# Kernel tuning notes

Hardware: AMD Instinct MI355X
Metric: run time of the kernel (lower is better)

The kernel has to match this reference:

```python
import jax, jax.numpy as jnp
import numpy as np

Z = 128          # z_size
K = 16           # number of objects
B = 2048         # batch size
DIM = 2 * Z      # 256


def _lin_init(k, out_dim, in_dim):
    bound = 1.0 / np.sqrt(in_dim)
    kw, kb = jax.random.split(k)
    W = jax.random.uniform(kw, (out_dim, in_dim), minval=-bound, maxval=bound, dtype=jnp.float32)
    b = jax.random.uniform(kb, (out_dim,), minval=-bound, maxval=bound, dtype=jnp.float32)
    return W, b


def setup_inputs() -> dict:
    key = jax.random.key(0)
    ks = jax.random.split(key, 12)
    W_obj, b_obj = _lin_init(ks[2], DIM, Z)            # d_obj: z_size -> dim
    Wih, bih = _lin_init(ks[3], 3 * Z, DIM)            # GRU input weights (dim -> z_size hidden)
    Whh, bhh = _lin_init(ks[4], 3 * Z, Z)              # GRU hidden weights
    We, be = _lin_init(ks[5], 2 * DIM, 2 * DIM)        # d_obj_eff: 512 -> 512
    Wa, ba = _lin_init(ks[6], 1, 2 * DIM)              # d_obj_att: 512 -> 1
    Wc, bc = _lin_init(ks[7], Z, DIM + 2 * DIM)        # d_comb: 768 -> z_size
    Wl, bl = _lin_init(ks[8], Z, Z)                    # loc
    Ws, bs = _lin_init(ks[9], Z, Z)                    # scale
    Wh, bh = _lin_init(ks[10], Z, Z)                   # h projection (RSSM)
    return {
        'z': jax.random.normal(ks[0], (B * K, Z), dtype=jnp.float32),
        'h0': jax.random.normal(ks[1], (B * K, Z), dtype=jnp.float32),
        'W_obj': W_obj, 'b_obj': b_obj,
        'Wih': Wih, 'bih': bih, 'Whh': Whh, 'bhh': bhh,
        'We': We, 'be': be, 'Wa': Wa, 'ba': ba,
        'Wc': Wc, 'bc': bc, 'Wl': Wl, 'bl': bl,
        'Ws': Ws, 'bs': bs, 'Wh': Wh, 'bh': bh,
    }


def _gru_step(x, h, Wih, Whh, bih, bhh):
    # torch nn.GRU single step, 1 layer
    gi = x @ Wih.T + bih
    gh = h @ Whh.T + bhh
    i_r, i_z, i_n = jnp.split(gi, 3, axis=-1)
    h_r, h_z, h_n = jnp.split(gh, 3, axis=-1)
    r = jax.nn.sigmoid(i_r + h_r)
    u = jax.nn.sigmoid(i_z + h_z)
    n = jnp.tanh(i_n + r * h_n)
    return (1.0 - u) * n + u * h


def reference(z, h0, W_obj, b_obj, Wih, bih, Whh, bhh, We, be, Wa, ba, Wc, bc, Wl, bl, Ws, bs, Wh, bh):
    # 1) object embedding
    z_embed = jax.nn.elu(z @ W_obj.T + b_obj)                      # [B*K, DIM]
    # 2) RSSM: one GRU step; output of step == new hidden for 1-layer GRU
    h_new = _gru_step(z_embed, h0, Wih, Whh, bih, bhh)             # [B*K, Z]
    ze = h_new.reshape(B, K, Z)
    z_emb = jnp.concatenate([ze, ze], axis=2)                      # [B, K, DIM] (output and hidden are identical)
    # 3) all unordered pairs i<j; effects are reused symmetrically
    ii, jj = np.triu_indices(K, k=1)                               # P = K*(K-1)/2 pairs
    zed = jnp.concatenate([z_emb[:, ii], z_emb[:, jj]], axis=-1)   # [B, P, 2*DIM]
    eff = jax.nn.elu(zed @ We.T + be)                              # [B, P, 2*DIM]
    att = jax.nn.sigmoid(eff @ Wa.T + ba)                          # [B, P, 1]
    w = att * eff                                                  # [B, P, 2*DIM]
    # 4) attention-weighted scatter-sum of effects to both endpoints
    E = jnp.zeros((B, K, 2 * DIM), dtype=w.dtype)
    E = E.at[:, ii].add(w).at[:, jj].add(w)                        # [B, K, 2*DIM]
    # 5) combine and project
    rel = (jnp.concatenate([z_emb, E], axis=-1) @ Wc.T + bc).reshape(B * K, Z)
    loc = rel @ Wl.T + bl
    scale = rel @ Ws.T + bs
    h_out = rel @ Wh.T + bh
    return (jnp.concatenate([loc, scale], axis=1), h_out)
```

## Files before the change

kernel.cpp:

```cpp
#include <hip/hip_runtime.h>


typedef __attribute__((ext_vector_type(8))) short bf16x8;
typedef __attribute__((ext_vector_type(4))) float f32x4;

__device__ __forceinline__ float fast_exp(float x) { return __expf(x); }
__device__ __forceinline__ float eluf(float x) {
  return x > 0.0f ? x : fast_exp(x) - 1.0f;
}
__device__ __forceinline__ float sigmoidf_(float x) {
  return __builtin_amdgcn_rcpf(1.0f + fast_exp(-x));
}
__device__ __forceinline__ float tanhf_(float x) {
  return 1.0f - 2.0f * __builtin_amdgcn_rcpf(fast_exp(2.0f * x) + 1.0f);
}
__device__ __forceinline__ short f2bf(float x) {
  unsigned u = __builtin_bit_cast(unsigned, x);
  unsigned r = (u + 0x7FFFu + ((u >> 16) & 1u)) >> 16;
  return (short)r;
}
__device__ __forceinline__ float bf2f(short s) {
  return __builtin_bit_cast(float, ((unsigned)(unsigned short)s) << 16);
}

__global__ __launch_bounds__(256) void prep_kernel(
    const float* __restrict__ We, const float* __restrict__ Wc,
    const float* __restrict__ Wl, const float* __restrict__ Wsc,
    const float* __restrict__ Wh, const float* __restrict__ bl,
    const float* __restrict__ bs, const float* __restrict__ bh,
    const float* __restrict__ W_obj, const float* __restrict__ Wih,
    const float* __restrict__ Whh,
    float* __restrict__ blsh, short* __restrict__ WUV2_bf,
    short* __restrict__ Wrel_bf, short* __restrict__ Wlsh_bf,
    short* __restrict__ Wobj_bf, short* __restrict__ Wih_bf,
    short* __restrict__ Whh_bf)
{
  int idx = blockIdx.x * 256 + threadIdx.x;
  if (idx < 131072) {
    int o = idx >> 7, d = idx & 127;
    float v;
    if (o < 512) v = We[o * 512 + d] + We[o * 512 + d + 128];
    else { int oo = o - 512; v = We[oo * 512 + d + 256] + We[oo * 512 + d + 384]; }
    WUV2_bf[idx] = f2bf(v);
  } else if (idx < 212992) {
    int j = idx - 131072; int o = j / 640, c = j - o * 640;
    float v = (c < 128) ? (Wc[o * 768 + c] + Wc[o * 768 + c + 128])
                        : Wc[o * 768 + c + 128];
    Wrel_bf[j] = f2bf(v);
  } else if (idx < 262144) {
    int j = idx - 212992; int o = j >> 7, c = j & 127;
    float v = (o < 128) ? Wl[o * 128 + c]
            : (o < 256) ? Wsc[(o - 128) * 128 + c]
                        : Wh[(o - 256) * 128 + c];
    Wlsh_bf[j] = f2bf(v);
  } else if (idx < 262528) {
    int j = idx - 262144;
    blsh[j] = (j < 128) ? bl[j] : (j < 256) ? bs[j - 128] : bh[j - 256];
  } else if (idx < 295296) {
    int j = idx - 262528; Wobj_bf[j] = f2bf(W_obj[j]);
  } else if (idx < 393600) {
    int j = idx - 295296; Wih_bf[j] = f2bf(Wih[j]);
  } else if (idx < 442752) {
    int j = idx - 393600; Whh_bf[j] = f2bf(Whh[j]);
  }
}

__global__ __launch_bounds__(256) void cvt_zh_kernel(
    const float* __restrict__ z, const float* __restrict__ h0,
    short* __restrict__ z_bf, short* __restrict__ h0_bf)
{
  int g = blockIdx.x * 256 + threadIdx.x;
  const float* src; short* dst; int off;
  if (g < 1048576) { src = z;  dst = z_bf;  off = g << 2; }
  else             { src = h0; dst = h0_bf; off = (g - 1048576) << 2; }
  float4 v = *(const float4*)(src + off);
  short4 o;
  o.x = f2bf(v.x); o.y = f2bf(v.y); o.z = f2bf(v.z); o.w = f2bf(v.w);
  *(short4*)(dst + off) = o;
}

template<int ACT, int OUTMODE, int HASBIAS>
__global__ __launch_bounds__(256) void mfma_gemm(
    const short* __restrict__ A, int lda, int K,
    const short* __restrict__ W,
    const float* __restrict__ bias,
    float* __restrict__ C, int ldc,
    short* __restrict__ Cb,
    float* __restrict__ C2)
{
  const int t = threadIdx.x;
  const int wv = t >> 6, l = t & 63;
  const int lr = l & 15, lk = l >> 4;
  const int row0 = blockIdx.x * 64 + wv * 16;
  const int col0 = blockIdx.y * 64;

  const short* Ap = A + (size_t)(row0 + lr) * lda + lk * 8;
  const short* Wp = W + (size_t)(col0 + lr) * K + lk * 8;
  const size_t wstep = (size_t)16 * K;

  f32x4 acc0 = {0.f,0.f,0.f,0.f}, acc1 = {0.f,0.f,0.f,0.f};
  f32x4 acc2 = {0.f,0.f,0.f,0.f}, acc3 = {0.f,0.f,0.f,0.f};
  for (int k0 = 0; k0 < K; k0 += 32) {
    bf16x8 a  = *(const bf16x8*)(Ap + k0);
    bf16x8 b0 = *(const bf16x8*)(Wp + k0);
    bf16x8 b1 = *(const bf16x8*)(Wp + wstep + k0);
    bf16x8 b2 = *(const bf16x8*)(Wp + 2 * wstep + k0);
    bf16x8 b3 = *(const bf16x8*)(Wp + 3 * wstep + k0);
    acc0 = __builtin_amdgcn_mfma_f32_16x16x32_bf16(a, b0, acc0, 0, 0, 0);
    acc1 = __builtin_amdgcn_mfma_f32_16x16x32_bf16(a, b1, acc1, 0, 0, 0);
    acc2 = __builtin_amdgcn_mfma_f32_16x16x32_bf16(a, b2, acc2, 0, 0, 0);
    acc3 = __builtin_amdgcn_mfma_f32_16x16x32_bf16(a, b3, acc3, 0, 0, 0);
  }
  f32x4 accs[4] = {acc0, acc1, acc2, acc3};
#pragma unroll
  for (int ct = 0; ct < 4; ++ct) {
    const int c = col0 + ct * 16 + lr;
    const float bv = HASBIAS ? bias[c] : 0.0f;
#pragma unroll
    for (int j = 0; j < 4; ++j) {
      const int r = row0 + lk * 4 + j;
      float x = accs[ct][j] + bv;
      if (ACT == 1) x = eluf(x);
      if (OUTMODE == 0) {
        C[(size_t)r * ldc + c] = x;
      } else if (OUTMODE == 1) {
        Cb[(size_t)r * ldc + c] = f2bf(x);
      } else {
        if (c < 256) C[(size_t)r * 256 + c] = x;
        else         C2[(size_t)r * 128 + (c - 256)] = x;
      }
    }
  }
}

__global__ __launch_bounds__(256) void gru_gates_kernel(
    const float* __restrict__ gi, const float* __restrict__ gh,
    const float* __restrict__ h0, short* __restrict__ Acat)
{
  int g = blockIdx.x * 256 + threadIdx.x;
  int r = g >> 5, c = (g & 31) << 2;
  const float* gir = gi + (size_t)r * 384;
  const float* ghr = gh + (size_t)r * 384;
  float4 ir  = *(const float4*)(gir + c);
  float4 iz  = *(const float4*)(gir + 128 + c);
  float4 in_ = *(const float4*)(gir + 256 + c);
  float4 hr  = *(const float4*)(ghr + c);
  float4 hz  = *(const float4*)(ghr + 128 + c);
  float4 hn  = *(const float4*)(ghr + 256 + c);
  float4 h   = *(const float4*)(h0 + (size_t)r * 128 + c);
  float4 o;
  {
    float rg = sigmoidf_(ir.x + hr.x), u = sigmoidf_(iz.x + hz.x);
    float n = tanhf_(in_.x + rg * hn.x);
    o.x = (1.f - u) * n + u * h.x;
  }
  {
    float rg = sigmoidf_(ir.y + hr.y), u = sigmoidf_(iz.y + hz.y);
    float n = tanhf_(in_.y + rg * hn.y);
    o.y = (1.f - u) * n + u * h.y;
  }
  {
    float rg = sigmoidf_(ir.z + hr.z), u = sigmoidf_(iz.z + hz.z);
    float n = tanhf_(in_.z + rg * hn.z);
    o.z = (1.f - u) * n + u * h.z;
  }
  {
    float rg = sigmoidf_(ir.w + hr.w), u = sigmoidf_(iz.w + hz.w);
    float n = tanhf_(in_.w + rg * hn.w);
    o.w = (1.f - u) * n + u * h.w;
  }
  short4 o4;
  o4.x = f2bf(o.x); o4.y = f2bf(o.y); o4.z = f2bf(o.z); o4.w = f2bf(o.w);
  *(short4*)(Acat + (size_t)r * 640 + c) = o4;
}

__global__ __launch_bounds__(512) void pair2_kernel(
    short* __restrict__ Acat,
    const float* __restrict__ UV_all,
    const float* __restrict__ be, const float* __restrict__ Wa,
    const float* __restrict__ ba)
{
  __shared__ float UV[16 * 1024];
  const int b = blockIdx.x, t = threadIdx.x;
  const int w = t >> 6, l = t & 63;

  {
    const float4* src = (const float4*)(UV_all + (size_t)b * 16384);
    float4* dst = (float4*)UV;
#pragma unroll
    for (int i = 0; i < 8; ++i) dst[t + i * 512] = src[t + i * 512];
  }
  float4 beA = *(const float4*)(be + (l << 2));
  float4 beB = *(const float4*)(be + 256 + (l << 2));
  float4 waA = *(const float4*)(Wa + (l << 2));
  float4 waB = *(const float4*)(Wa + 256 + (l << 2));
  const float ba0 = ba[0];
  __syncthreads();

#pragma unroll
  for (int kk = 0; kk < 2; ++kk) {
    const int k = (w << 1) + kk;
    float accA[4] = {0.f, 0.f, 0.f, 0.f};
    float accB[4] = {0.f, 0.f, 0.f, 0.f};
#pragma unroll 1
    for (int m = 0; m < 16; ++m) {
      if (m == k) continue;
      int i = k < m ? k : m;
      int j = k < m ? m : k;
      const float* Ui = &UV[i * 1024 + (l << 2)];
      const float* Vj = &UV[j * 1024 + 512 + (l << 2)];
      float4 u0 = *(const float4*)Ui;
      float4 u1 = *(const float4*)(Ui + 256);
      float4 v0 = *(const float4*)Vj;
      float4 v1 = *(const float4*)(Vj + 256);
      float eA[4], eB[4];
      eA[0] = eluf(u0.x + v0.x + beA.x);
      eA[1] = eluf(u0.y + v0.y + beA.y);
      eA[2] = eluf(u0.z + v0.z + beA.z);
      eA[3] = eluf(u0.w + v0.w + beA.w);
      eB[0] = eluf(u1.x + v1.x + beB.x);
      eB[1] = eluf(u1.y + v1.y + beB.y);
      eB[2] = eluf(u1.z + v1.z + beB.z);
      eB[3] = eluf(u1.w + v1.w + beB.w);
      float s;
      s = eA[0] * waA.x;
      s = fmaf(eA[1], waA.y, s);
      s = fmaf(eA[2], waA.z, s);
      s = fmaf(eA[3], waA.w, s);
      s = fmaf(eB[0], waB.x, s);
      s = fmaf(eB[1], waB.y, s);
      s = fmaf(eB[2], waB.z, s);
      s = fmaf(eB[3], waB.w, s);
#pragma unroll
      for (int off = 1; off < 64; off <<= 1) s += __shfl_xor(s, off, 64);
      float att = sigmoidf_(s + ba0);
      accA[0] = fmaf(att, eA[0], accA[0]);
      accA[1] = fmaf(att, eA[1], accA[1]);
      accA[2] = fmaf(att, eA[2], accA[2]);
      accA[3] = fmaf(att, eA[3], accA[3]);
      accB[0] = fmaf(att, eB[0], accB[0]);
      accB[1] = fmaf(att, eB[1], accB[1]);
      accB[2] = fmaf(att, eB[2], accB[2]);
      accB[3] = fmaf(att, eB[3], accB[3]);
    }
    short* dst = Acat + (size_t)(b * 16 + k) * 640 + 128;
    short4 oA, oB;
    oA.x = f2bf(accA[0]); oA.y = f2bf(accA[1]);
    oA.z = f2bf(accA[2]); oA.w = f2bf(accA[3]);
    oB.x = f2bf(accB[0]); oB.y = f2bf(accB[1]);
    oB.z = f2bf(accB[2]); oB.w = f2bf(accB[3]);
    *(short4*)(dst + (l << 2)) = oA;
    *(short4*)(dst + 256 + (l << 2)) = oB;
  }
}

extern "C" void kernel_launch(void* const* d_in, const int* in_sizes, int n_in,
                              void* d_out, int out_size, void* d_ws, size_t ws_size,
                              hipStream_t stream)
{
  (void)in_sizes; (void)n_in; (void)out_size; (void)ws_size;
  const float* z     = (const float*)d_in[0];
  const float* h0    = (const float*)d_in[1];
  const float* W_obj = (const float*)d_in[2];
  const float* b_obj = (const float*)d_in[3];
  const float* Wih   = (const float*)d_in[4];
  const float* bih   = (const float*)d_in[5];
  const float* Whh   = (const float*)d_in[6];
  const float* bhh   = (const float*)d_in[7];
  const float* We    = (const float*)d_in[8];
  const float* be    = (const float*)d_in[9];
  const float* Wa    = (const float*)d_in[10];
  const float* ba    = (const float*)d_in[11];
  const float* Wc    = (const float*)d_in[12];
  const float* bc    = (const float*)d_in[13];
  const float* Wl    = (const float*)d_in[14];
  const float* bl    = (const float*)d_in[15];
  const float* Wsc   = (const float*)d_in[16];
  const float* bs    = (const float*)d_in[17];
  const float* Wh    = (const float*)d_in[18];
  const float* bh    = (const float*)d_in[19];

  float* ws  = (float*)d_ws;
  float* out = (float*)d_out;

  float* gi     = ws;
  float* gh     = ws + 12582912;
  float* UV_all = ws;
  float* blsh   = ws + 33554432;
  short* bfb    = (short*)(ws + 33554816);
  short* z_bf    = bfb;
  short* h0_bf   = bfb + 4194304;
  short* x_bf    = bfb + 8388608;
  short* Acat_bf = bfb + 16777216;
  short* rel_bf  = bfb + 37748736;
  short* Wobj_bf = bfb + 41943040;
  short* Wih_bf  = bfb + 41975808;
  short* Whh_bf  = bfb + 42074112;
  short* Wrel_bf = bfb + 42123264;
  short* Wlsh_bf = bfb + 42205184;
  short* WUV2_bf = bfb + 42254336;

  prep_kernel<<<1730, 256, 0, stream>>>(We, Wc, Wl, Wsc, Wh, bl, bs, bh,
                                        W_obj, Wih, Whh,
                                        blsh, WUV2_bf, Wrel_bf, Wlsh_bf,
                                        Wobj_bf, Wih_bf, Whh_bf);
  cvt_zh_kernel<<<8192, 256, 0, stream>>>(z, h0, z_bf, h0_bf);
  mfma_gemm<1, 1, 1><<<dim3(512, 4), 256, 0, stream>>>(
      z_bf, 128, 128, Wobj_bf, b_obj, nullptr, 256, x_bf, nullptr);
  mfma_gemm<0, 0, 1><<<dim3(512, 6), 256, 0, stream>>>(
      x_bf, 256, 256, Wih_bf, bih, gi, 384, nullptr, nullptr);
  mfma_gemm<0, 0, 1><<<dim3(512, 6), 256, 0, stream>>>(
      h0_bf, 128, 128, Whh_bf, bhh, gh, 384, nullptr, nullptr);
  gru_gates_kernel<<<4096, 256, 0, stream>>>(gi, gh, h0, Acat_bf);
  mfma_gemm<0, 0, 0><<<dim3(512, 16), 256, 0, stream>>>(
      Acat_bf, 640, 128, WUV2_bf, nullptr, UV_all, 1024, nullptr, nullptr);
  pair2_kernel<<<2048, 512, 0, stream>>>(Acat_bf, UV_all, be, Wa, ba);
  mfma_gemm<0, 1, 1><<<dim3(512, 2), 256, 0, stream>>>(
      Acat_bf, 640, 640, Wrel_bf, bc, nullptr, 128, rel_bf, nullptr);
  mfma_gemm<0, 2, 1><<<dim3(512, 6), 256, 0, stream>>>(
      rel_bf, 128, 128, Wlsh_bf, blsh, out, 0, nullptr, out + 8388608);
}
```

Baseline: 509.0 us.

## Fuse GRU gate GEMMs with gate math and compute UV projection inside pair kernel

Replaces the two GRU GEMMs and the separate gate kernel with one kernel that computes the input and hidden gate projections through MFMA and applies the gate nonlinearities in registers. This removes the fp32 gi/gh intermediates. The UV projection GEMM is also moved into pair2_kernel, so each batch block computes its 16x1024 UV tile directly into shared memory instead of reading a 64MB fp32 buffer from global memory. The cost is lower parallelism in the GRU kernel, which runs only 512 blocks with an 8-iteration serial column loop. There are also more redundant weight loads per block.

```diff
diff --git a/kernel.cpp b/kernel.cpp
--- a/kernel.cpp
+++ b/kernel.cpp
@@ -18,9 +18,6 @@
   unsigned u = __builtin_bit_cast(unsigned, x);
   unsigned r = (u + 0x7FFFu + ((u >> 16) & 1u)) >> 16;
   return (short)r;
-}
-__device__ __forceinline__ float bf2f(short s) {
-  return __builtin_bit_cast(float, ((unsigned)(unsigned short)s) << 16);
 }
 
 __global__ __launch_bounds__(256) void prep_kernel(
@@ -79,7 +76,7 @@
   *(short4*)(dst + off) = o;
 }
 
-template<int ACT, int OUTMODE, int HASBIAS>
+template<int ACT, int OUTMODE>
 __global__ __launch_bounds__(256) void mfma_gemm(
     const short* __restrict__ A, int lda, int K,
     const short* __restrict__ W,
@@ -115,7 +112,7 @@
 #pragma unroll
   for (int ct = 0; ct < 4; ++ct) {
     const int c = col0 + ct * 16 + lr;
-    const float bv = HASBIAS ? bias[c] : 0.0f;
+    const float bv = bias[c];
 #pragma unroll
     for (int j = 0; j < 4; ++j) {
       const int r = row0 + lk * 4 + j;
@@ -133,62 +130,95 @@
   }
 }
 
-__global__ __launch_bounds__(256) void gru_gates_kernel(
-    const float* __restrict__ gi, const float* __restrict__ gh,
-    const float* __restrict__ h0, short* __restrict__ Acat)
-{
-  int g = blockIdx.x * 256 + threadIdx.x;
-  int r = g >> 5, c = (g & 31) << 2;
-  const float* gir = gi + (size_t)r * 384;
-  const float* ghr = gh + (size_t)r * 384;
-  float4 ir  = *(const float4*)(gir + c);
-  float4 iz  = *(const float4*)(gir + 128 + c);
-  float4 in_ = *(const float4*)(gir + 256 + c);
-  float4 hr  = *(const float4*)(ghr + c);
-  float4 hz  = *(const float4*)(ghr + 128 + c);
-  float4 hn  = *(const float4*)(ghr + 256 + c);
-  float4 h   = *(const float4*)(h0 + (size_t)r * 128 + c);
-  float4 o;
-  {
-    float rg = sigmoidf_(ir.x + hr.x), u = sigmoidf_(iz.x + hz.x);
-    float n = tanhf_(in_.x + rg * hn.x);
-    o.x = (1.f - u) * n + u * h.x;
-  }
-  {
-    float rg = sigmoidf_(ir.y + hr.y), u = sigmoidf_(iz.y + hz.y);
-    float n = tanhf_(in_.y + rg * hn.y);
-    o.y = (1.f - u) * n + u * h.y;
-  }
-  {
-    float rg = sigmoidf_(ir.z + hr.z), u = sigmoidf_(iz.z + hz.z);
-    float n = tanhf_(in_.z + rg * hn.z);
-    o.z = (1.f - u) * n + u * h.z;
-  }
-  {
-    float rg = sigmoidf_(ir.w + hr.w), u = sigmoidf_(iz.w + hz.w);
-    float n = tanhf_(in_.w + rg * hn.w);
-    o.w = (1.f - u) * n + u * h.w;
-  }
-  short4 o4;
-  o4.x = f2bf(o.x); o4.y = f2bf(o.y); o4.z = f2bf(o.z); o4.w = f2bf(o.w);
-  *(short4*)(Acat + (size_t)r * 640 + c) = o4;
+__global__ __launch_bounds__(256) void gru_fused(
+    const short* __restrict__ x_bf,
+    const short* __restrict__ h0_bf,
+    const float* __restrict__ h0,
+    const short* __restrict__ Wih_bf,
+    const short* __restrict__ Whh_bf,
+    const float* __restrict__ bih, const float* __restrict__ bhh,
+    short* __restrict__ Acat)
+{
+  const int t = threadIdx.x;
+  const int wv = t >> 6, l = t & 63;
+  const int lr = l & 15, lk = l >> 4;
+  const int row0 = blockIdx.x * 64 + wv * 16;
+
+  const short* Ax = x_bf + (size_t)(row0 + lr) * 256 + lk * 8;
+  const short* Ah = h0_bf + (size_t)(row0 + lr) * 128 + lk * 8;
+  bf16x8 ax[8], ah[4];
+#pragma unroll
+  for (int s = 0; s < 8; ++s) ax[s] = *(const bf16x8*)(Ax + s * 32);
+#pragma unroll
+  for (int s = 0; s < 4; ++s) ah[s] = *(const bf16x8*)(Ah + s * 32);
+
+#pragma unroll 1
+  for (int ct = 0; ct < 8; ++ct) {
+    const int c = ct * 16 + lr;
+    f32x4 gir = {0.f,0.f,0.f,0.f}, giz = {0.f,0.f,0.f,0.f}, gin = {0.f,0.f,0.f,0.f};
+    f32x4 ghr = {0.f,0.f,0.f,0.f}, ghz = {0.f,0.f,0.f,0.f}, ghn = {0.f,0.f,0.f,0.f};
+    const short* Wi0 = Wih_bf + (size_t)(c) * 256 + lk * 8 - lr * 256 + lr * 256;
+    const short* Wir = Wih_bf + (size_t)(ct * 16 + lr) * 256 + lk * 8;
+    const short* Wiz = Wih_bf + (size_t)(128 + ct * 16 + lr) * 256 + lk * 8;
+    const short* Win = Wih_bf + (size_t)(256 + ct * 16 + lr) * 256 + lk * 8;
+    (void)Wi0;
+#pragma unroll
+    for (int s = 0; s < 8; ++s) {
+      gir = __builtin_amdgcn_mfma_f32_16x16x32_bf16(ax[s], *(const bf16x8*)(Wir + s * 32), gir, 0, 0, 0);
+      giz = __builtin_amdgcn_mfma_f32_16x16x32_bf16(ax[s], *(const bf16x8*)(Wiz + s * 32), giz, 0, 0, 0);
+      gin = __builtin_amdgcn_mfma_f32_16x16x32_bf16(ax[s], *(const bf16x8*)(Win + s * 32), gin, 0, 0, 0);
+    }
+    const short* Whr = Whh_bf + (size_t)(ct * 16 + lr) * 128 + lk * 8;
+    const short* Whz = Whh_bf + (size_t)(128 + ct * 16 + lr) * 128 + lk * 8;
+    const short* Whn = Whh_bf + (size_t)(256 + ct * 16 + lr) * 128 + lk * 8;
+#pragma unroll
+    for (int s = 0; s < 4; ++s) {
+      ghr = __builtin_amdgcn_mfma_f32_16x16x32_bf16(ah[s], *(const bf16x8*)(Whr + s * 32), ghr, 0, 0, 0);
+      ghz = __builtin_amdgcn_mfma_f32_16x16x32_bf16(ah[s], *(const bf16x8*)(Whz + s * 32), ghz, 0, 0, 0);
+      ghn = __builtin_amdgcn_mfma_f32_16x16x32_bf16(ah[s], *(const bf16x8*)(Whn + s * 32), ghn, 0, 0, 0);
+    }
+    const float br = bih[c], bz = bih[c + 128], bn = bih[c + 256];
+    const float cr = bhh[c], cz = bhh[c + 128], cn = bhh[c + 256];
+#pragma unroll
+    for (int j = 0; j < 4; ++j) {
+      const int r = row0 + lk * 4 + j;
+      float rg = sigmoidf_((gir[j] + br) + (ghr[j] + cr));
+      float u  = sigmoidf_((giz[j] + bz) + (ghz[j] + cz));
+      float n  = tanhf_((gin[j] + bn) + rg * (ghn[j] + cn));
+      float hv = h0[(size_t)r * 128 + c];
+      Acat[(size_t)r * 640 + c] = f2bf((1.f - u) * n + u * hv);
+    }
+  }
 }
 
 __global__ __launch_bounds__(512) void pair2_kernel(
     short* __restrict__ Acat,
-    const float* __restrict__ UV_all,
+    const short* __restrict__ WUV2_bf,
     const float* __restrict__ be, const float* __restrict__ Wa,
     const float* __restrict__ ba)
 {
   __shared__ float UV[16 * 1024];
   const int b = blockIdx.x, t = threadIdx.x;
   const int w = t >> 6, l = t & 63;
+  const int lr = l & 15, lk = l >> 4;
 
   {
-    const float4* src = (const float4*)(UV_all + (size_t)b * 16384);
-    float4* dst = (float4*)UV;
-#pragma unroll
-    for (int i = 0; i < 8; ++i) dst[t + i * 512] = src[t + i * 512];
+    const short* Ap = Acat + (size_t)(b * 16 + lr) * 640 + lk * 8;
+    bf16x8 ah[4];
+#pragma unroll
+    for (int s = 0; s < 4; ++s) ah[s] = *(const bf16x8*)(Ap + s * 32);
+#pragma unroll
+    for (int ct = 0; ct < 8; ++ct) {
+      const int col0 = w * 128 + ct * 16;
+      const short* Wp = WUV2_bf + (size_t)(col0 + lr) * 128 + lk * 8;
+      f32x4 acc = {0.f, 0.f, 0.f, 0.f};
+#pragma unroll
+      for (int s = 0; s < 4; ++s)
+        acc = __builtin_amdgcn_mfma_f32_16x16x32_bf16(ah[s], *(const bf16x8*)(Wp + s * 32), acc, 0, 0, 0);
+#pragma unroll
+      for (int j = 0; j < 4; ++j)
+        UV[(lk * 4 + j) * 1024 + col0 + lr] = acc[j];
+    }
   }
   float4 beA = *(const float4*)(be + (l << 2));
   float4 beB = *(const float4*)(be + 256 + (l << 2));
@@ -283,11 +313,8 @@
   float* ws  = (float*)d_ws;
   float* out = (float*)d_out;
 
-  float* gi     = ws;
-  float* gh     = ws + 12582912;
-  float* UV_all = ws;
-  float* blsh   = ws + 33554432;
-  short* bfb    = (short*)(ws + 33554816);
+  float* blsh = ws;
+  short* bfb  = (short*)(ws + 384);
   short* z_bf    = bfb;
   short* h0_bf   = bfb + 4194304;
   short* x_bf    = bfb + 8388608;
@@ -305,18 +332,13 @@
                                         blsh, WUV2_bf, Wrel_bf, Wlsh_bf,
                                         Wobj_bf, Wih_bf, Whh_bf);
   cvt_zh_kernel<<<8192, 256, 0, stream>>>(z, h0, z_bf, h0_bf);
-  mfma_gemm<1, 1, 1><<<dim3(512, 4), 256, 0, stream>>>(
+  mfma_gemm<1, 1><<<dim3(512, 4), 256, 0, stream>>>(
       z_bf, 128, 128, Wobj_bf, b_obj, nullptr, 256, x_bf, nullptr);
-  mfma_gemm<0, 0, 1><<<dim3(512, 6), 256, 0, stream>>>(
-      x_bf, 256, 256, Wih_bf, bih, gi, 384, nullptr, nullptr);
-  mfma_gemm<0, 0, 1><<<dim3(512, 6), 256, 0, stream>>>(
-      h0_bf, 128, 128, Whh_bf, bhh, gh, 384, nullptr, nullptr);
-  gru_gates_kernel<<<4096, 256, 0, stream>>>(gi, gh, h0, Acat_bf);
-  mfma_gemm<0, 0, 0><<<dim3(512, 16), 256, 0, stream>>>(
-      Acat_bf, 640, 128, WUV2_bf, nullptr, UV_all, 1024, nullptr, nullptr);
-  pair2_kernel<<<2048, 512, 0, stream>>>(Acat_bf, UV_all, be, Wa, ba);
-  mfma_gemm<0, 1, 1><<<dim3(512, 2), 256, 0, stream>>>(
+  gru_fused<<<512, 256, 0, stream>>>(x_bf, h0_bf, h0, Wih_bf, Whh_bf,
+                                     bih, bhh, Acat_bf);
+  pair2_kernel<<<2048, 512, 0, stream>>>(Acat_bf, WUV2_bf, be, Wa, ba);
+  mfma_gemm<0, 1><<<dim3(512, 2), 256, 0, stream>>>(
       Acat_bf, 640, 640, Wrel_bf, bc, nullptr, 128, rel_bf, nullptr);
-  mfma_gemm<0, 2, 1><<<dim3(512, 6), 256, 0, stream>>>(
+  mfma_gemm<0, 2><<<dim3(512, 6), 256, 0, stream>>>(
       rel_bf, 128, 128, Wlsh_bf, blsh, out, 0, nullptr, out + 8388608);
 }
```

Result: faster. 411.1 us (-19.2%).
